# Kernel tuning notes

Hardware: AMD Instinct MI355X
Metric: run time of the kernel (lower is better)

The kernel has to match this reference:

```python
import jax, jax.numpy as jnp
import numpy as np

B, S, DIM, H = 2, 2048, 1024, 16
DH = DIM // H            # 64
G = DH // 4              # 16 quaternion groups per head
IQ = DIM // 4            # 256
ROPE_BASE = 10000.0
SCALE = DH ** -0.5


def qlinear(x, wr, wi, wj, wk, b):
    # x: [B,S,4*IQ]; strided quaternion components, exact combo from QuaternionLinear.forward
    xr, xi, xj, xk = x[..., 0::4], x[..., 1::4], x[..., 2::4], x[..., 3::4]
    o_r = xr @ wr.T - xi @ wi.T - xj @ wj.T - xk @ wk.T
    o_i = xi @ wr.T + xr @ wi.T + xk @ wk.T - xj @ wj.T
    o_j = xj @ wr.T - xk @ wk.T + xr @ wj.T + xi @ wi.T
    o_k = xk @ wr.T + xj @ wj.T - xi @ wi.T + xr @ wk.T
    out = jnp.stack([o_r, o_i, o_j, o_k], axis=-1).reshape(x.shape[:-1] + (-1,))
    return out + b


def qrope(x):
    # x: [B,H,S,DH]; left quaternion multiply u(theta) \otimes q, axis_mode='cycle'
    b, h, s, dh = x.shape
    g = dh // 4
    xq = x.reshape(b, h, s, g, 4)
    t = jnp.arange(s, dtype=x.dtype)
    inv = 1.0 / (ROPE_BASE ** (jnp.arange(g, dtype=x.dtype) / g))
    ang = t[:, None] * inv[None, :]            # [S,G]
    cos, sin = jnp.cos(ang), jnp.sin(ang)
    gi = jnp.arange(g)
    ax_i = (gi % 3 == 0).astype(x.dtype)
    ax_j = (gi % 3 == 1).astype(x.dtype)
    ax_k = (gi % 3 == 2).astype(x.dtype)
    ur, ui, uj, uk = cos, sin * ax_i, sin * ax_j, sin * ax_k   # [S,G] broadcast over [B,H,S,G]
    xr, xi, xj, xk = xq[..., 0], xq[..., 1], xq[..., 2], xq[..., 3]
    pr = ur * xr - ui * xi - uj * xj - uk * xk
    pi = ur * xi + ui * xr + uj * xk - uk * xj
    pj = ur * xj - ui * xk + uj * xr + uk * xi
    pk = ur * xk + ui * xj - uj * xi + uk * xr
    return jnp.stack([pr, pi, pj, pk], axis=-1).reshape(b, h, s, dh)


def setup_inputs() -> dict:
    key = jax.random.key(0)
    ks = jax.random.split(key, 24)
    x = jax.random.normal(ks[0], (B, S, DIM), dtype=jnp.float32)
    # causal mask: True = masked
    mask = jnp.broadcast_to(jnp.triu(jnp.ones((S, S), dtype=bool), k=1), (B, S, S))
    inp = {"x": x, "mask": mask}
    i = 1
    for proj in ("q", "k", "v", "o"):
        for comp in ("wr", "wi", "wj", "wk"):
            inp[f"{proj}_{comp}"] = jax.random.normal(ks[i], (IQ, IQ), dtype=jnp.float32) * 0.02
            i += 1
        inp[f"{proj}_b"] = jnp.zeros((DIM,), dtype=jnp.float32)
    return inp


def reference(x, mask,
              q_wr, q_wi, q_wj, q_wk, q_b,
              k_wr, k_wi, k_wj, k_wk, k_b,
              v_wr, v_wi, v_wj, v_wk, v_b,
              o_wr, o_wi, o_wj, o_wk, o_b):
    b, s, dm = x.shape
    q = qlinear(x, q_wr, q_wi, q_wj, q_wk, q_b).reshape(b, s, H, DH).transpose(0, 2, 1, 3)
    k = qlinear(x, k_wr, k_wi, k_wj, k_wk, k_b).reshape(b, s, H, DH).transpose(0, 2, 1, 3)
    v = qlinear(x, v_wr, v_wi, v_wj, v_wk, v_b).reshape(b, s, H, DH).transpose(0, 2, 1, 3)
    q, k = qrope(q), qrope(k)
    scores = jnp.einsum('bhsd,bhtd->bhst', q, k) * SCALE
    scores = jnp.where(mask[:, None, :, :], -jnp.inf, scores)
    a = jax.nn.softmax(scores, axis=-1)
    out = jnp.einsum('bhst,bhtd->bhsd', a, v).transpose(0, 2, 1, 3).reshape(b, s, dm)
    return qlinear(out, o_wr, o_wi, o_wj, o_wk, o_b)
```

## Files before the change

### kernel.cpp

```cpp
#include <hip/hip_runtime.h>
#include <stdint.h>

typedef unsigned short u16;
typedef unsigned int   u32;

#define NB   2
#define NS   2048
#define NDIM 1024
#define NH   16
#define NDH  64
#define QSCALE 0.18033688011112042f

typedef __bf16 bf16x8 __attribute__((ext_vector_type(8)));
typedef float  f32x4  __attribute__((ext_vector_type(4)));

#define MFMA_BF16(a,b,c) __builtin_amdgcn_mfma_f32_16x16x32_bf16((a),(b),(c),0,0,0)

#define XBF_OFF   (256)
#define WD_OFF    (XBF_OFF  + 8*1024*1024)
#define BIAS_OFF  (WD_OFF   + 8*1024*1024)
#define QB_OFF    (BIAS_OFF + 16384)
#define KB_OFF    (QB_OFF   + 8*1024*1024)
#define VT_OFF    (KB_OFF   + 8*1024*1024)
#define OP_OFF    (VT_OFF   + 8*1024*1024)
#define LP_OFF    (OP_OFF   + 16*1024*1024)

__device__ __forceinline__ float bf2f(u16 h){
  union { u32 u; float f; } v; v.u = ((u32)h) << 16; return v.f;
}
__device__ __forceinline__ u16 f2bf(float f){
  union { float f; u32 u; } v; v.f = f;
  u32 r = (v.u >> 16) & 1u;
  return (u16)((v.u + 0x7fffu + r) >> 16);
}
__device__ __forceinline__ float load_val(const void* p, int i, int isbf){
  return isbf ? bf2f(((const u16*)p)[i]) : ((const float*)p)[i];
}
__device__ __forceinline__ void gl_lds16(const u16* g, u16* l){
  __builtin_amdgcn_global_load_lds(
      (__attribute__((address_space(1))) void*)(uintptr_t)g,
      (__attribute__((address_space(3))) void*)(uintptr_t)l,
      16, 0, 0);
}

__global__ void detect_kernel(const u16* __restrict__ x, int* __restrict__ flag){
  __shared__ int cnt;
  if (threadIdx.x == 0) cnt = 0;
  __syncthreads();
  int ok = 0;
  int base = threadIdx.x * 16;
  for (int i = base; i < base + 16; ++i){
    u16 h = x[i];
    int e = (h >> 7) & 0xFF;
    if ((e > 96 && e < 158) || ((h & 0x7FFF) == 0)) ok++;
  }
  atomicAdd(&cnt, ok);
  __syncthreads();
  if (threadIdx.x == 0) *flag = (cnt > 3600) ? 1 : 0;
}

__global__ void conv_x_kernel(const void* __restrict__ xin, u16* __restrict__ xbf,
                              const int* __restrict__ flag){
  int isbf = *flag;
  int t = blockIdx.x * 256 + threadIdx.x;
  if (isbf){
    ((uint4*)xbf)[t] = ((const uint4*)xin)[t];
  } else {
    const float4* f4 = (const float4*)xin;
    float4 a = f4[2*t], b = f4[2*t+1];
    ushort4 lo = { f2bf(a.x), f2bf(a.y), f2bf(a.z), f2bf(a.w) };
    ushort4 hi = { f2bf(b.x), f2bf(b.y), f2bf(b.z), f2bf(b.w) };
    ((ushort4*)xbf)[2*t]   = lo;
    ((ushort4*)xbf)[2*t+1] = hi;
  }
}

struct QPtrs { const void* w[16]; const void* b[4]; };

__global__ void build_w_kernel(QPtrs ptrs, u16* __restrict__ wd,
                               float* __restrict__ biasf, const int* __restrict__ flag){
  int isbf = *flag;
  int idx = blockIdx.x * 256 + threadIdx.x;
  int n = idx & 255, m = (idx >> 8) & 255, c = (idx >> 16) & 3, p = idx >> 18;
  int src = m * 256 + n;
  float vr = load_val(ptrs.w[p*4+0], src, isbf);
  float vi = load_val(ptrs.w[p*4+1], src, isbf);
  float vj = load_val(ptrs.w[p*4+2], src, isbf);
  float vk = load_val(ptrs.w[p*4+3], src, isbf);
  float o0, o1, o2, o3;
  switch (c){
    case 0:  o0 = vr; o1 = -vi; o2 = -vj; o3 = -vk; break;
    case 1:  o0 = vi; o1 =  vr; o2 = -vj; o3 =  vk; break;
    case 2:  o0 = vj; o1 =  vi; o2 =  vr; o3 = -vk; break;
    default: o0 = vk; o1 = -vi; o2 =  vj; o3 =  vr; break;
  }
  ushort4 sv = { f2bf(o0), f2bf(o1), f2bf(o2), f2bf(o3) };
  *(ushort4*)&wd[(size_t)p * 1048576 + (size_t)(4*m + c) * 1024 + 4*n] = sv;
  if (idx < 4096){
    int pp = idx >> 10, oo = idx & 1023;
    biasf[idx] = load_val(ptrs.b[pp], oo, isbf);
  }
}

__global__ __launch_bounds__(256)
void gemm_qkv_kernel(const u16* __restrict__ A, const u16* __restrict__ Bw,
                     const float* __restrict__ bias,
                     u16* __restrict__ qb, u16* __restrict__ kb, u16* __restrict__ vt){
  __shared__ u16 sA[2][128 * 32];
  __shared__ u16 sB[2][128 * 32];
  int tid = threadIdx.x, w = tid >> 6, lane = tid & 63, quad = lane >> 4, l16 = lane & 15;
  int n0 = blockIdx.x * 128, m0 = blockIdx.y * 128;

  f32x4 acc[4][4];
#pragma unroll
  for (int i = 0; i < 4; ++i)
#pragma unroll
    for (int j = 0; j < 4; ++j) acc[i][j] = (f32x4){0.f, 0.f, 0.f, 0.f};

  int cp = lane & 3, rl = lane >> 2;
  int gc = (cp ^ ((rl >> 1) & 3)) * 8;
  const u16* ga = A  + (size_t)(m0 + w*16 + rl) * 1024 + gc;
  const u16* gb = Bw + (size_t)(n0 + w*16 + rl) * 1024 + gc;
  int ldo = w * 512 + lane * 8;
  int xorv = ((l16 >> 1) & 3) * 8;
  int mw = (w & 1) * 64, nw = (w >> 1) * 64;

  auto stage = [&](int k0, int b){
#pragma unroll
    for (int i = 0; i < 2; ++i){
      gl_lds16(ga + (size_t)i * 65536 + k0, &sA[b][ldo + i * 2048]);
      gl_lds16(gb + (size_t)i * 65536 + k0, &sB[b][ldo + i * 2048]);
    }
  };

  stage(0, 0);
  for (int it = 0; it < 32; ++it){
    __syncthreads();
    if (it < 31) stage((it + 1) * 32, (it + 1) & 1);
    const u16* cA = sA[it & 1];
    const u16* cB = sB[it & 1];
    bf16x8 af[4], bfr[4];
#pragma unroll
    for (int mt = 0; mt < 4; ++mt)
      af[mt] = *(const bf16x8*)&cA[(mw + mt*16 + l16) * 32 + (quad*8 ^ xorv)];
#pragma unroll
    for (int nt = 0; nt < 4; ++nt)
      bfr[nt] = *(const bf16x8*)&cB[(nw + nt*16 + l16) * 32 + (quad*8 ^ xorv)];
#pragma unroll
    for (int mt = 0; mt < 4; ++mt)
#pragma unroll
      for (int nt = 0; nt < 4; ++nt)
        acc[mt][nt] = MFMA_BF16(af[mt], bfr[nt], acc[mt][nt]);
  }

  int proj = n0 >> 10;
  if (proj == 2){
#pragma unroll
    for (int mt = 0; mt < 4; ++mt){
      int row = m0 + mw + mt*16 + quad*4;
      int b = row >> 11, seq0 = row & 2047;
#pragma unroll
      for (int nt = 0; nt < 4; ++nt){
        int col = n0 + nw + nt*16 + l16;
        int o = col & 1023, h = o >> 6, d = o & 63;
        float bv = bias[col];
        ushort4 pv = { f2bf(acc[mt][nt][0] + bv), f2bf(acc[mt][nt][1] + bv),
                       f2bf(acc[mt][nt][2] + bv), f2bf(acc[mt][nt][3] + bv) };
        *(ushort4*)&vt[((size_t)((b*16 + h) * 64 + d)) * 2048 + seq0] = pv;
      }
    }
  } else {
    float sc = (proj == 0) ? QSCALE : 1.0f;
    u16* dst = proj ? kb : qb;
    int c = l16 & 3;
#pragma unroll
    for (int nt = 0; nt < 4; ++nt){
      int col = n0 + nw + nt*16 + l16;
      int o = col & 1023, h = o >> 6, d = o & 63;
      int g = d >> 2;
      int ax = g % 3;
      int mask = ax + 1;
      int tbl = (ax == 0) ? 0xA : (ax == 1 ? 0x6 : 0xC);
      float sgn = ((tbl >> c) & 1) ? 1.f : -1.f;
      float inv = __builtin_amdgcn_exp2f(-(float)g * 0.8304820237218405f);
      float bv = bias[col];
#pragma unroll
      for (int mt = 0; mt < 4; ++mt){
        int row0 = m0 + mw + mt*16 + quad*4;
        int b = row0 >> 11, s0 = row0 & 2047;
        size_t obase = ((size_t)((b*16 + h) * 2048 + s0)) * 64 + d;
#pragma unroll
        for (int r = 0; r < 4; ++r){
          float v = acc[mt][nt][r] + bv;
          float vp = __shfl_xor(v, mask);
          float ang = (float)(s0 + r) * inv;
          float co = __cosf(ang) * sc;
          float si = __sinf(ang) * sc * sgn;
          dst[obase + (size_t)r * 64] = f2bf(co * v + si * vp);
        }
      }
    }
  }
}

__global__ __launch_bounds__(256)
void gemm_o_kernel(const u16* __restrict__ A, const u16* __restrict__ Bw,
                   const float* __restrict__ bias, void* __restrict__ dout,
                   const int* __restrict__ flag){
  __shared__ u16 sA[2][64 * 32];
  __shared__ u16 sB[2][128 * 32];
  int tid = threadIdx.x, w = tid >> 6, lane = tid & 63, quad = lane >> 4, l16 = lane & 15;
  int n0 = blockIdx.x * 128, m0 = blockIdx.y * 64;

  f32x4 acc[2][4];
#pragma unroll
  for (int i = 0; i < 2; ++i)
#pragma unroll
    for (int j = 0; j < 4; ++j) acc[i][j] = (f32x4){0.f, 0.f, 0.f, 0.f};

  int cp = lane & 3, rl = lane >> 2;
  int gc = (cp ^ ((rl >> 1) & 3)) * 8;
  int xorv = ((l16 >> 1) & 3) * 8;
  int mw = (w & 1) * 32, nw = (w >> 1) * 64;

  auto stage = [&](int k0, int b){
#pragma unroll
    for (int i = 0; i < 3; ++i){
      int ch = w * 3 + i;
      int lr = (ch < 4 ? ch : ch - 4) * 16 + rl;
      int eo = (ch < 4 ? ch : ch - 4) * 512 + lane * 8;
      if (ch < 4) gl_lds16(A  + (size_t)(m0 + lr) * 1024 + k0 + gc, &sA[b][eo]);
      else        gl_lds16(Bw + (size_t)(n0 + lr) * 1024 + k0 + gc, &sB[b][eo]);
    }
  };

  stage(0, 0);
  for (int it = 0; it < 32; ++it){
    __syncthreads();
    if (it < 31) stage((it + 1) * 32, (it + 1) & 1);
    const u16* cA = sA[it & 1];
    const u16* cB = sB[it & 1];
    bf16x8 af[2], bfr[4];
#pragma unroll
    for (int mt = 0; mt < 2; ++mt)
      af[mt] = *(const bf16x8*)&cA[(mw + mt*16 + l16) * 32 + (quad*8 ^ xorv)];
#pragma unroll
    for (int nt = 0; nt < 4; ++nt)
      bfr[nt] = *(const bf16x8*)&cB[(nw + nt*16 + l16) * 32 + (quad*8 ^ xorv)];
#pragma unroll
    for (int mt = 0; mt < 2; ++mt)
#pragma unroll
      for (int nt = 0; nt < 4; ++nt)
        acc[mt][nt] = MFMA_BF16(af[mt], bfr[nt], acc[mt][nt]);
  }

  int isbf = *flag;
#pragma unroll
  for (int mt = 0; mt < 2; ++mt){
    int row = m0 + mw + mt*16 + quad*4;
#pragma unroll
    for (int nt = 0; nt < 4; ++nt){
      int col = n0 + nw + nt*16 + l16;
      float bv = bias[col];
#pragma unroll
      for (int r = 0; r < 4; ++r){
        float val = acc[mt][nt][r] + bv;
        size_t addr = (size_t)(row + r) * 1024 + col;
        if (isbf) ((u16*)dout)[addr] = f2bf(val);
        else      ((float*)dout)[addr] = val;
      }
    }
  }
}

#define SPT 20

__global__ __launch_bounds__(256, 3)
void attn_kernel(const u16* __restrict__ Q, const u16* __restrict__ K,
                 const u16* __restrict__ Vt, u16* __restrict__ OP,
                 float* __restrict__ LP){
  __shared__ u16 sK[2][4096];
  __shared__ u16 sPT[4][64 * SPT];
  int bh  = blockIdx.x;
  int spl = blockIdx.y;
  int qt  = 15 - (int)blockIdx.z;
  int tid = threadIdx.x, w = tid >> 6, lane = tid & 63, quad = lane >> 4, l16 = lane & 15;
  size_t kbase = (size_t)bh * 2048 * 64;
  size_t vbase = (size_t)bh * 64 * 2048;
  int rowbase = qt * 128 + w * 32;
  u16* spw = &sPT[w][0];

  bf16x8 qf[2][2];
#pragma unroll
  for (int g = 0; g < 2; ++g)
#pragma unroll
    for (int kc = 0; kc < 2; ++kc)
      qf[g][kc] = *(const bf16x8*)(Q + kbase + (size_t)(rowbase + g*16 + l16) * 64 + kc*32 + quad*8);

  f32x4 oaccT[2][4];
  float lsum[2][4];
#pragma unroll
  for (int g = 0; g < 2; ++g)
#pragma unroll
    for (int i = 0; i < 4; ++i){ oaccT[g][i] = (f32x4){0.f,0.f,0.f,0.f}; lsum[g][i] = 0.f; }

  int kt0 = spl ? (qt + 1) : 0;
  int ntiles = qt + 1;

  auto stage = [&](int kt, int b){
    int kcol = kt * 64;
#pragma unroll
    for (int p = 0; p < 2; ++p){
      int slot = w*128 + p*64 + lane;
      int row = slot >> 3, dc = (slot & 7) ^ (row & 7);
      gl_lds16(K + kbase + (size_t)(kcol + row) * 64 + dc*8, &sK[b][(w*128 + p*64) * 8]);
    }
  };

  stage(kt0, 0);
  for (int i = 0; i < ntiles; ++i){
    int kcol = (kt0 + i) * 64;
    __syncthreads();
    if (i + 1 < ntiles) stage(kt0 + i + 1, (i + 1) & 1);
    const u16* bK = sK[i & 1];

    if (kcol <= rowbase + 31){
      bf16x8 vf[4][2];
#pragma unroll
      for (int dn = 0; dn < 4; ++dn)
#pragma unroll
        for (int kc = 0; kc < 2; ++kc)
          vf[dn][kc] = *(const bf16x8*)(Vt + vbase + (size_t)(dn*16 + l16) * 2048
                                        + kcol + kc*32 + quad*8);
      bf16x8 bk[2][4];
#pragma unroll
      for (int kc = 0; kc < 2; ++kc)
#pragma unroll
        for (int nt = 0; nt < 4; ++nt){
          int rw = nt*16 + l16;
          int ch = ((kc*4 + quad) ^ (rw & 7)) * 8;
          bk[kc][nt] = *(const bf16x8*)&bK[rw*64 + ch];
        }
#pragma unroll
      for (int g = 0; g < 2; ++g){
        int G0 = rowbase + g*16;
        if (kcol <= G0 + 15){
          f32x4 sacc[4];
#pragma unroll
          for (int nt = 0; nt < 4; ++nt) sacc[nt] = (f32x4){0.f,0.f,0.f,0.f};
#pragma unroll
          for (int kc = 0; kc < 2; ++kc)
#pragma unroll
            for (int nt = 0; nt < 4; ++nt)
              sacc[nt] = MFMA_BF16(qf[g][kc], bk[kc][nt], sacc[nt]);

          if (kcol + 63 > G0){
#pragma unroll
            for (int nt = 0; nt < 4; ++nt){
              int col = kcol + nt*16 + l16;
              ushort4 pv;
#pragma unroll
              for (int r = 0; r < 4; ++r){
                int row = G0 + quad*4 + r;
                float pp = (col <= row) ? __builtin_amdgcn_exp2f(sacc[nt][r]) : 0.f;
                lsum[g][r] += pp;
                ((u16*)&pv)[r] = f2bf(pp);
              }
              *(ushort4*)&spw[(nt*16 + l16) * SPT + quad*4] = pv;
            }
          } else {
#pragma unroll
            for (int nt = 0; nt < 4; ++nt){
              ushort4 pv;
#pragma unroll
              for (int r = 0; r < 4; ++r){
                float pp = __builtin_amdgcn_exp2f(sacc[nt][r]);
                lsum[g][r] += pp;
                ((u16*)&pv)[r] = f2bf(pp);
              }
              *(ushort4*)&spw[(nt*16 + l16) * SPT + quad*4] = pv;
            }
          }
#pragma unroll
          for (int kc = 0; kc < 2; ++kc){
            bf16x8 pf;
#pragma unroll
            for (int j = 0; j < 8; ++j)
              pf[j] = ((const __bf16*)spw)[(kc*32 + quad*8 + j) * SPT + l16];
#pragma unroll
            for (int dn = 0; dn < 4; ++dn)
              oaccT[g][dn] = MFMA_BF16(vf[dn][kc], pf, oaccT[g][dn]);
          }
        }
      }
    }
  }

  float* scr = (float*)spw;
#pragma unroll
  for (int g = 0; g < 2; ++g)
#pragma unroll
    for (int r = 0; r < 4; ++r){
      float l = lsum[g][r];
      l += __shfl_xor(l, 1); l += __shfl_xor(l, 2);
      l += __shfl_xor(l, 4); l += __shfl_xor(l, 8);
      if (l16 == 0) scr[g*16 + quad*4 + r] = l;
    }
  float lrow[2];
#pragma unroll
  for (int g = 0; g < 2; ++g) lrow[g] = scr[g*16 + l16];

  size_t obase = ((size_t)(spl*32 + bh)) * 2048;
#pragma unroll
  for (int g = 0; g < 2; ++g){
    int row = rowbase + g*16 + l16;
    if (quad == 0) LP[obase + row] = lrow[g];
#pragma unroll
    for (int dn = 0; dn < 4; ++dn){
      ushort4 ov = { f2bf(oaccT[g][dn][0]), f2bf(oaccT[g][dn][1]),
                     f2bf(oaccT[g][dn][2]), f2bf(oaccT[g][dn][3]) };
      *(ushort4*)&OP[(obase + row) * 64 + dn*16 + quad*4] = ov;
    }
  }
}

__global__ void combine_kernel(const u16* __restrict__ OP, const float* __restrict__ LP,
                               u16* __restrict__ Ab){
  int idx = blockIdx.x * 256 + threadIdx.x;
  int dc = idx & 7, s = (idx >> 3) & 2047, bh = idx >> 14;
  size_t r0 = (size_t)bh * 2048 + s, r1 = (size_t)(32 + bh) * 2048 + s;
  float invl = 1.f / (LP[r0] + LP[r1]);
  union { uint4 v; u16 h[8]; } a0, a1; ushort4 o[2];
  a0.v = *(const uint4*)&OP[r0 * 64 + dc*8];
  a1.v = *(const uint4*)&OP[r1 * 64 + dc*8];
#pragma unroll
  for (int p = 0; p < 2; ++p)
#pragma unroll
    for (int j = 0; j < 4; ++j)
      ((u16*)&o[p])[j] = f2bf((bf2f(a0.h[p*4+j]) + bf2f(a1.h[p*4+j])) * invl);
  int b = bh >> 4, h = bh & 15;
  u16* dst = &Ab[((size_t)(b*2048 + s)) * 1024 + h*64 + dc*8];
  *(ushort4*)dst = o[0];
  *(ushort4*)(dst + 4) = o[1];
}

extern "C" void kernel_launch(void* const* d_in, const int* in_sizes, int n_in,
                              void* d_out, int out_size, void* d_ws, size_t ws_size,
                              hipStream_t stream){
  (void)in_sizes; (void)n_in; (void)out_size; (void)ws_size;
  char* ws = (char*)d_ws;
  int*   flag  = (int*)ws;
  u16*   Xbf   = (u16*)(ws + XBF_OFF);
  u16*   Wd    = (u16*)(ws + WD_OFF);
  float* biasf = (float*)(ws + BIAS_OFF);
  u16*   Qb    = (u16*)(ws + QB_OFF);
  u16*   Kb    = (u16*)(ws + KB_OFF);
  u16*   Vt    = (u16*)(ws + VT_OFF);
  u16*   OP    = (u16*)(ws + OP_OFF);
  float* LP    = (float*)(ws + LP_OFF);
  u16*   Ab    = Xbf;

  detect_kernel<<<1, 256, 0, stream>>>((const u16*)d_in[0], flag);
  conv_x_kernel<<<2048, 256, 0, stream>>>(d_in[0], Xbf, flag);

  QPtrs ptrs;
  for (int p = 0; p < 4; ++p){
    for (int wi = 0; wi < 4; ++wi) ptrs.w[p*4 + wi] = d_in[2 + p*5 + wi];
    ptrs.b[p] = d_in[2 + p*5 + 4];
  }
  build_w_kernel<<<4096, 256, 0, stream>>>(ptrs, Wd, biasf, flag);

  gemm_qkv_kernel<<<dim3(24, 32), 256, 0, stream>>>(Xbf, Wd, biasf, Qb, Kb, Vt);
  attn_kernel<<<dim3(32, 2, 16), 256, 0, stream>>>(Qb, Kb, Vt, OP, LP);
  combine_kernel<<<2048, 256, 0, stream>>>(OP, LP, Ab);
  gemm_o_kernel<<<dim3(8, 64), 256, 0, stream>>>(Ab, Wd + 3*1048576, biasf + 3072,
                                                 d_out, flag);
}
```

Measured before the change: 254.3 us.

## Shrink GEMM tiles and load A fragments directly from global into registers

Both the QKV and output-projection GEMMs now use smaller M (and for O, N) tiles and double the grid size, with launch bounds raised to 4 blocks per SU. The A operand is no longer staged through LDS. Each wave loads its own MFMA A-fragment straight from global memory into registers and prefetches the next k-step into a second register set, while B stays double-buffered in LDS. The aim is more blocks for latency hiding and less LDS traffic and space, at the cost of less data reuse per tile and A reads that go uncoalesced or repeat across waves.

Result: slower. 284.4 us (+11.8%).

```diff
diff --git a/kernel.cpp b/kernel.cpp
--- a/kernel.cpp
+++ b/kernel.cpp
@@ -102,61 +102,68 @@
   }
 }
 
-__global__ __launch_bounds__(256)
+__global__ __launch_bounds__(256, 4)
 void gemm_qkv_kernel(const u16* __restrict__ A, const u16* __restrict__ Bw,
                      const float* __restrict__ bias,
                      u16* __restrict__ qb, u16* __restrict__ kb, u16* __restrict__ vt){
-  __shared__ u16 sA[2][128 * 32];
   __shared__ u16 sB[2][128 * 32];
   int tid = threadIdx.x, w = tid >> 6, lane = tid & 63, quad = lane >> 4, l16 = lane & 15;
-  int n0 = blockIdx.x * 128, m0 = blockIdx.y * 128;
-
-  f32x4 acc[4][4];
-#pragma unroll
-  for (int i = 0; i < 4; ++i)
+  int n0 = blockIdx.x * 128, m0 = blockIdx.y * 64;
+
+  f32x4 acc[2][4];
+#pragma unroll
+  for (int i = 0; i < 2; ++i)
 #pragma unroll
     for (int j = 0; j < 4; ++j) acc[i][j] = (f32x4){0.f, 0.f, 0.f, 0.f};
 
   int cp = lane & 3, rl = lane >> 2;
   int gc = (cp ^ ((rl >> 1) & 3)) * 8;
-  const u16* ga = A  + (size_t)(m0 + w*16 + rl) * 1024 + gc;
-  const u16* gb = Bw + (size_t)(n0 + w*16 + rl) * 1024 + gc;
-  int ldo = w * 512 + lane * 8;
   int xorv = ((l16 >> 1) & 3) * 8;
-  int mw = (w & 1) * 64, nw = (w >> 1) * 64;
-
-  auto stage = [&](int k0, int b){
+  int mw = (w & 1) * 32, nw = (w >> 1) * 64;
+
+  const u16* ga0 = A + (size_t)(m0 + mw + l16) * 1024 + quad * 8;
+
+  auto stageB = [&](int k0, int b){
 #pragma unroll
     for (int i = 0; i < 2; ++i){
-      gl_lds16(ga + (size_t)i * 65536 + k0, &sA[b][ldo + i * 2048]);
-      gl_lds16(gb + (size_t)i * 65536 + k0, &sB[b][ldo + i * 2048]);
+      int ch = w * 2 + i;
+      gl_lds16(Bw + (size_t)(n0 + ch*16 + rl) * 1024 + k0 + gc,
+               &sB[b][ch * 512 + lane * 8]);
     }
   };
 
-  stage(0, 0);
+  bf16x8 afc[2], afn[2];
+  stageB(0, 0);
+#pragma unroll
+  for (int mt = 0; mt < 2; ++mt)
+    afc[mt] = *(const bf16x8*)(ga0 + (size_t)mt * 16384);
+
   for (int it = 0; it < 32; ++it){
     __syncthreads();
-    if (it < 31) stage((it + 1) * 32, (it + 1) & 1);
-    const u16* cA = sA[it & 1];
+    if (it < 31){
+      stageB((it + 1) * 32, (it + 1) & 1);
+#pragma unroll
+      for (int mt = 0; mt < 2; ++mt)
+        afn[mt] = *(const bf16x8*)(ga0 + (size_t)mt * 16384 + (it + 1) * 32);
+    }
     const u16* cB = sB[it & 1];
-    bf16x8 af[4], bfr[4];
-#pragma unroll
-    for (int mt = 0; mt < 4; ++mt)
-      af[mt] = *(const bf16x8*)&cA[(mw + mt*16 + l16) * 32 + (quad*8 ^ xorv)];
+    bf16x8 bfr[4];
 #pragma unroll
     for (int nt = 0; nt < 4; ++nt)
       bfr[nt] = *(const bf16x8*)&cB[(nw + nt*16 + l16) * 32 + (quad*8 ^ xorv)];
 #pragma unroll
-    for (int mt = 0; mt < 4; ++mt)
+    for (int mt = 0; mt < 2; ++mt)
 #pragma unroll
       for (int nt = 0; nt < 4; ++nt)
-        acc[mt][nt] = MFMA_BF16(af[mt], bfr[nt], acc[mt][nt]);
+        acc[mt][nt] = MFMA_BF16(afc[mt], bfr[nt], acc[mt][nt]);
+#pragma unroll
+    for (int mt = 0; mt < 2; ++mt) afc[mt] = afn[mt];
   }
 
   int proj = n0 >> 10;
   if (proj == 2){
 #pragma unroll
-    for (int mt = 0; mt < 4; ++mt){
+    for (int mt = 0; mt < 2; ++mt){
       int row = m0 + mw + mt*16 + quad*4;
       int b = row >> 11, seq0 = row & 2047;
 #pragma unroll
@@ -185,7 +192,7 @@
       float inv = __builtin_amdgcn_exp2f(-(float)g * 0.8304820237218405f);
       float bv = bias[col];
 #pragma unroll
-      for (int mt = 0; mt < 4; ++mt){
+      for (int mt = 0; mt < 2; ++mt){
         int row0 = m0 + mw + mt*16 + quad*4;
         int b = row0 >> 11, s0 = row0 & 2047;
         size_t obase = ((size_t)((b*16 + h) * 2048 + s0)) * 64 + d;
@@ -203,55 +210,58 @@
   }
 }
 
-__global__ __launch_bounds__(256)
+__global__ __launch_bounds__(256, 4)
 void gemm_o_kernel(const u16* __restrict__ A, const u16* __restrict__ Bw,
                    const float* __restrict__ bias, void* __restrict__ dout,
                    const int* __restrict__ flag){
-  __shared__ u16 sA[2][64 * 32];
-  __shared__ u16 sB[2][128 * 32];
+  __shared__ u16 sB[2][64 * 32];
   int tid = threadIdx.x, w = tid >> 6, lane = tid & 63, quad = lane >> 4, l16 = lane & 15;
-  int n0 = blockIdx.x * 128, m0 = blockIdx.y * 64;
-
-  f32x4 acc[2][4];
+  int n0 = blockIdx.x * 64, m0 = blockIdx.y * 64;
+
+  f32x4 acc[2][2];
 #pragma unroll
   for (int i = 0; i < 2; ++i)
 #pragma unroll
-    for (int j = 0; j < 4; ++j) acc[i][j] = (f32x4){0.f, 0.f, 0.f, 0.f};
+    for (int j = 0; j < 2; ++j) acc[i][j] = (f32x4){0.f, 0.f, 0.f, 0.f};
 
   int cp = lane & 3, rl = lane >> 2;
   int gc = (cp ^ ((rl >> 1) & 3)) * 8;
   int xorv = ((l16 >> 1) & 3) * 8;
-  int mw = (w & 1) * 32, nw = (w >> 1) * 64;
-
-  auto stage = [&](int k0, int b){
-#pragma unroll
-    for (int i = 0; i < 3; ++i){
-      int ch = w * 3 + i;
-      int lr = (ch < 4 ? ch : ch - 4) * 16 + rl;
-      int eo = (ch < 4 ? ch : ch - 4) * 512 + lane * 8;
-      if (ch < 4) gl_lds16(A  + (size_t)(m0 + lr) * 1024 + k0 + gc, &sA[b][eo]);
-      else        gl_lds16(Bw + (size_t)(n0 + lr) * 1024 + k0 + gc, &sB[b][eo]);
-    }
+  int mw = (w & 1) * 32, nw = (w >> 1) * 32;
+
+  const u16* ga0 = A + (size_t)(m0 + mw + l16) * 1024 + quad * 8;
+
+  auto stageB = [&](int k0, int b){
+    gl_lds16(Bw + (size_t)(n0 + w*16 + rl) * 1024 + k0 + gc,
+             &sB[b][w * 512 + lane * 8]);
   };
 
-  stage(0, 0);
+  bf16x8 afc[2], afn[2];
+  stageB(0, 0);
+#pragma unroll
+  for (int mt = 0; mt < 2; ++mt)
+    afc[mt] = *(const bf16x8*)(ga0 + (size_t)mt * 16384);
+
   for (int it = 0; it < 32; ++it){
     __syncthreads();
-    if (it < 31) stage((it + 1) * 32, (it + 1) & 1);
-    const u16* cA = sA[it & 1];
+    if (it < 31){
+      stageB((it + 1) * 32, (it + 1) & 1);
+#pragma unroll
+      for (int mt = 0; mt < 2; ++mt)
+        afn[mt] = *(const bf16x8*)(ga0 + (size_t)mt * 16384 + (it + 1) * 32);
+    }
     const u16* cB = sB[it & 1];
-    bf16x8 af[2], bfr[4];
+    bf16x8 bfr[2];
+#pragma unroll
+    for (int nt = 0; nt < 2; ++nt)
+      bfr[nt] = *(const bf16x8*)&cB[(nw + nt*16 + l16) * 32 + (quad*8 ^ xorv)];
 #pragma unroll
     for (int mt = 0; mt < 2; ++mt)
-      af[mt] = *(const bf16x8*)&cA[(mw + mt*16 + l16) * 32 + (quad*8 ^ xorv)];
-#pragma unroll
-    for (int nt = 0; nt < 4; ++nt)
-      bfr[nt] = *(const bf16x8*)&cB[(nw + nt*16 + l16) * 32 + (quad*8 ^ xorv)];
-#pragma unroll
-    for (int mt = 0; mt < 2; ++mt)
-#pragma unroll
-      for (int nt = 0; nt < 4; ++nt)
-        acc[mt][nt] = MFMA_BF16(af[mt], bfr[nt], acc[mt][nt]);
+#pragma unroll
+      for (int nt = 0; nt < 2; ++nt)
+        acc[mt][nt] = MFMA_BF16(afc[mt], bfr[nt], acc[mt][nt]);
+#pragma unroll
+    for (int mt = 0; mt < 2; ++mt) afc[mt] = afn[mt];
   }
 
   int isbf = *flag;
@@ -259,7 +269,7 @@
   for (int mt = 0; mt < 2; ++mt){
     int row = m0 + mw + mt*16 + quad*4;
 #pragma unroll
-    for (int nt = 0; nt < 4; ++nt){
+    for (int nt = 0; nt < 2; ++nt){
       int col = n0 + nw + nt*16 + l16;
       float bv = bias[col];
 #pragma unroll
@@ -470,9 +480,9 @@
   }
   build_w_kernel<<<4096, 256, 0, stream>>>(ptrs, Wd, biasf, flag);
 
-  gemm_qkv_kernel<<<dim3(24, 32), 256, 0, stream>>>(Xbf, Wd, biasf, Qb, Kb, Vt);
+  gemm_qkv_kernel<<<dim3(24, 64), 256, 0, stream>>>(Xbf, Wd, biasf, Qb, Kb, Vt);
   attn_kernel<<<dim3(32, 2, 16), 256, 0, stream>>>(Qb, Kb, Vt, OP, LP);
   combine_kernel<<<2048, 256, 0, stream>>>(OP, LP, Ab);
-  gemm_o_kernel<<<dim3(8, 64), 256, 0, stream>>>(Ab, Wd + 3*1048576, biasf + 3072,
-                                                 d_out, flag);
-}
+  gemm_o_kernel<<<dim3(16, 64), 256, 0, stream>>>(Ab, Wd + 3*1048576, biasf + 3072,
+                                                  d_out, flag);
+}
```

## Load QKV GEMM fragments directly from global memory into registers, dropping LDS staging

Applied to the files above, without the earlier changes.

Replaces the LDS double-buffered tiles in the QKV projection GEMM with direct global loads of MFMA fragments into registers, prefetching the next k-step while the current one computes. This removes the per-iteration __syncthreads and the LDS traffic. In exchange, data is no longer shared across waves, so each A/B row is fetched by two waves from global/L2. The per-lane 16-byte loads are also less coalesced than before, and register pressure goes up.

New measurement: 297.7 us. +17.1%, slower.

```diff
diff --git a/kernel.cpp b/kernel.cpp
--- a/kernel.cpp
+++ b/kernel.cpp
@@ -106,10 +106,9 @@
 void gemm_qkv_kernel(const u16* __restrict__ A, const u16* __restrict__ Bw,
                      const float* __restrict__ bias,
                      u16* __restrict__ qb, u16* __restrict__ kb, u16* __restrict__ vt){
-  __shared__ u16 sA[2][128 * 32];
-  __shared__ u16 sB[2][128 * 32];
   int tid = threadIdx.x, w = tid >> 6, lane = tid & 63, quad = lane >> 4, l16 = lane & 15;
   int n0 = blockIdx.x * 128, m0 = blockIdx.y * 128;
+  int mw = (w & 1) * 64, nw = (w >> 1) * 64;
 
   f32x4 acc[4][4];
 #pragma unroll
@@ -117,40 +116,33 @@
 #pragma unroll
     for (int j = 0; j < 4; ++j) acc[i][j] = (f32x4){0.f, 0.f, 0.f, 0.f};
 
-  int cp = lane & 3, rl = lane >> 2;
-  int gc = (cp ^ ((rl >> 1) & 3)) * 8;
-  const u16* ga = A  + (size_t)(m0 + w*16 + rl) * 1024 + gc;
-  const u16* gb = Bw + (size_t)(n0 + w*16 + rl) * 1024 + gc;
-  int ldo = w * 512 + lane * 8;
-  int xorv = ((l16 >> 1) & 3) * 8;
-  int mw = (w & 1) * 64, nw = (w >> 1) * 64;
-
-  auto stage = [&](int k0, int b){
-#pragma unroll
-    for (int i = 0; i < 2; ++i){
-      gl_lds16(ga + (size_t)i * 65536 + k0, &sA[b][ldo + i * 2048]);
-      gl_lds16(gb + (size_t)i * 65536 + k0, &sB[b][ldo + i * 2048]);
-    }
-  };
-
-  stage(0, 0);
+  const u16* pa = A  + (size_t)(m0 + mw + l16) * 1024 + quad * 8;
+  const u16* pb = Bw + (size_t)(n0 + nw + l16) * 1024 + quad * 8;
+
+  bf16x8 afc[4], bfc[4], afn[4], bfn[4];
+#pragma unroll
+  for (int t = 0; t < 4; ++t){
+    afc[t] = *(const bf16x8*)(pa + (size_t)t * 16384);
+    bfc[t] = *(const bf16x8*)(pb + (size_t)t * 16384);
+  }
+
+#pragma unroll 2
   for (int it = 0; it < 32; ++it){
-    __syncthreads();
-    if (it < 31) stage((it + 1) * 32, (it + 1) & 1);
-    const u16* cA = sA[it & 1];
-    const u16* cB = sB[it & 1];
-    bf16x8 af[4], bfr[4];
+    if (it < 31){
+      int k1 = (it + 1) * 32;
+#pragma unroll
+      for (int t = 0; t < 4; ++t){
+        afn[t] = *(const bf16x8*)(pa + (size_t)t * 16384 + k1);
+        bfn[t] = *(const bf16x8*)(pb + (size_t)t * 16384 + k1);
+      }
+    }
 #pragma unroll
     for (int mt = 0; mt < 4; ++mt)
-      af[mt] = *(const bf16x8*)&cA[(mw + mt*16 + l16) * 32 + (quad*8 ^ xorv)];
-#pragma unroll
-    for (int nt = 0; nt < 4; ++nt)
-      bfr[nt] = *(const bf16x8*)&cB[(nw + nt*16 + l16) * 32 + (quad*8 ^ xorv)];
-#pragma unroll
-    for (int mt = 0; mt < 4; ++mt)
 #pragma unroll
       for (int nt = 0; nt < 4; ++nt)
-        acc[mt][nt] = MFMA_BF16(af[mt], bfr[nt], acc[mt][nt]);
+        acc[mt][nt] = MFMA_BF16(afc[mt], bfc[nt], acc[mt][nt]);
+#pragma unroll
+    for (int t = 0; t < 4; ++t){ afc[t] = afn[t]; bfc[t] = bfn[t]; }
   }
 
   int proj = n0 >> 10;
```

## Fuse split-attention combine into output GEMM and merge prep kernels

Applied to the files above, without the earlier changes.

Folds the detect, convert-x and build-weight kernels into one prep kernel that does per-block dtype detection, removing two launches and a serial detection pass. Also removes the combine kernel: the output-projection GEMM now reads the two partial attention outputs and their row sums directly, normalises them while staging its A tile into padded LDS, and so skips an intermediate activation round-trip through memory. The price is that A staging in the GEMM becomes register-mediated global loads plus ALU work instead of async global-to-LDS copies, and 8 GEMM column blocks redo the same combine for each row tile.

New measurement: 259.3 us. No clear change (+2.0%).

```diff
diff --git a/kernel.cpp b/kernel.cpp
--- a/kernel.cpp
+++ b/kernel.cpp
@@ -42,63 +42,68 @@
       (__attribute__((address_space(3))) void*)(uintptr_t)l,
       16, 0, 0);
 }
-
-__global__ void detect_kernel(const u16* __restrict__ x, int* __restrict__ flag){
+__device__ __forceinline__ int sane16(u16 h){
+  int e = (h >> 7) & 0xFF;
+  return ((e > 96 && e < 158) || ((h & 0x7FFF) == 0)) ? 1 : 0;
+}
+
+struct QPtrs { const void* w[16]; const void* b[4]; };
+
+__global__ void prep_kernel(const void* __restrict__ xin, u16* __restrict__ xbf,
+                            QPtrs ptrs, u16* __restrict__ wd,
+                            float* __restrict__ biasf, int* __restrict__ flag){
   __shared__ int cnt;
-  if (threadIdx.x == 0) cnt = 0;
+  int bx = blockIdx.x, tid = threadIdx.x;
+  if (tid == 0) cnt = 0;
   __syncthreads();
-  int ok = 0;
-  int base = threadIdx.x * 16;
-  for (int i = base; i < base + 16; ++i){
-    u16 h = x[i];
-    int e = (h >> 7) & 0xFF;
-    if ((e > 96 && e < 158) || ((h & 0x7FFF) == 0)) ok++;
-  }
-  atomicAdd(&cnt, ok);
-  __syncthreads();
-  if (threadIdx.x == 0) *flag = (cnt > 3600) ? 1 : 0;
-}
-
-__global__ void conv_x_kernel(const void* __restrict__ xin, u16* __restrict__ xbf,
-                              const int* __restrict__ flag){
-  int isbf = *flag;
-  int t = blockIdx.x * 256 + threadIdx.x;
-  if (isbf){
-    ((uint4*)xbf)[t] = ((const uint4*)xin)[t];
+
+  if (bx < 2048){
+    int t = bx * 256 + tid;
+    uint4 v = ((const uint4*)xin)[t];
+    const u16* hv = (const u16*)&v;
+    int ok = 0;
+#pragma unroll
+    for (int j = 0; j < 8; ++j) ok += sane16(hv[j]);
+    atomicAdd(&cnt, ok);
+    __syncthreads();
+    int isbf = (cnt > 1700) ? 1 : 0;
+    if (bx == 0 && tid == 0) *flag = isbf;
+    if (isbf){
+      ((uint4*)xbf)[t] = v;
+    } else {
+      const float4* f4 = (const float4*)xin;
+      float4 a = f4[2*t], b = f4[2*t+1];
+      ushort4 lo = { f2bf(a.x), f2bf(a.y), f2bf(a.z), f2bf(a.w) };
+      ushort4 hi = { f2bf(b.x), f2bf(b.y), f2bf(b.z), f2bf(b.w) };
+      ((ushort4*)xbf)[2*t]   = lo;
+      ((ushort4*)xbf)[2*t+1] = hi;
+    }
   } else {
-    const float4* f4 = (const float4*)xin;
-    float4 a = f4[2*t], b = f4[2*t+1];
-    ushort4 lo = { f2bf(a.x), f2bf(a.y), f2bf(a.z), f2bf(a.w) };
-    ushort4 hi = { f2bf(b.x), f2bf(b.y), f2bf(b.z), f2bf(b.w) };
-    ((ushort4*)xbf)[2*t]   = lo;
-    ((ushort4*)xbf)[2*t+1] = hi;
-  }
-}
-
-struct QPtrs { const void* w[16]; const void* b[4]; };
-
-__global__ void build_w_kernel(QPtrs ptrs, u16* __restrict__ wd,
-                               float* __restrict__ biasf, const int* __restrict__ flag){
-  int isbf = *flag;
-  int idx = blockIdx.x * 256 + threadIdx.x;
-  int n = idx & 255, m = (idx >> 8) & 255, c = (idx >> 16) & 3, p = idx >> 18;
-  int src = m * 256 + n;
-  float vr = load_val(ptrs.w[p*4+0], src, isbf);
-  float vi = load_val(ptrs.w[p*4+1], src, isbf);
-  float vj = load_val(ptrs.w[p*4+2], src, isbf);
-  float vk = load_val(ptrs.w[p*4+3], src, isbf);
-  float o0, o1, o2, o3;
-  switch (c){
-    case 0:  o0 = vr; o1 = -vi; o2 = -vj; o3 = -vk; break;
-    case 1:  o0 = vi; o1 =  vr; o2 = -vj; o3 =  vk; break;
-    case 2:  o0 = vj; o1 =  vi; o2 =  vr; o3 = -vk; break;
-    default: o0 = vk; o1 = -vi; o2 =  vj; o3 =  vr; break;
-  }
-  ushort4 sv = { f2bf(o0), f2bf(o1), f2bf(o2), f2bf(o3) };
-  *(ushort4*)&wd[(size_t)p * 1048576 + (size_t)(4*m + c) * 1024 + 4*n] = sv;
-  if (idx < 4096){
-    int pp = idx >> 10, oo = idx & 1023;
-    biasf[idx] = load_val(ptrs.b[pp], oo, isbf);
+    int idx = (bx - 2048) * 256 + tid;
+    int n = idx & 255, m = (idx >> 8) & 255, c = (idx >> 16) & 3, p = idx >> 18;
+    const u16* probe = (const u16*)ptrs.w[p*4];
+    int ok = sane16(probe[tid]) + sane16(probe[tid + 256]);
+    atomicAdd(&cnt, ok);
+    __syncthreads();
+    int isbf = (cnt > 450) ? 1 : 0;
+    int src = m * 256 + n;
+    float vr = load_val(ptrs.w[p*4+0], src, isbf);
+    float vi = load_val(ptrs.w[p*4+1], src, isbf);
+    float vj = load_val(ptrs.w[p*4+2], src, isbf);
+    float vk = load_val(ptrs.w[p*4+3], src, isbf);
+    float o0, o1, o2, o3;
+    switch (c){
+      case 0:  o0 = vr; o1 = -vi; o2 = -vj; o3 = -vk; break;
+      case 1:  o0 = vi; o1 =  vr; o2 = -vj; o3 =  vk; break;
+      case 2:  o0 = vj; o1 =  vi; o2 =  vr; o3 = -vk; break;
+      default: o0 = vk; o1 = -vi; o2 =  vj; o3 =  vr; break;
+    }
+    ushort4 sv = { f2bf(o0), f2bf(o1), f2bf(o2), f2bf(o3) };
+    *(ushort4*)&wd[(size_t)p * 1048576 + (size_t)(4*m + c) * 1024 + 4*n] = sv;
+    if (idx < 4096){
+      int pp = idx >> 10, oo = idx & 1023;
+      biasf[idx] = load_val(ptrs.b[pp], oo, isbf);
+    }
   }
 }
 
@@ -204,10 +209,10 @@
 }
 
 __global__ __launch_bounds__(256)
-void gemm_o_kernel(const u16* __restrict__ A, const u16* __restrict__ Bw,
-                   const float* __restrict__ bias, void* __restrict__ dout,
-                   const int* __restrict__ flag){
-  __shared__ u16 sA[2][64 * 32];
+void gemm_o_kernel(const u16* __restrict__ OP, const float* __restrict__ LP,
+                   const u16* __restrict__ Bw, const float* __restrict__ bias,
+                   void* __restrict__ dout, const int* __restrict__ flag){
+  __shared__ u16 sA[2][64 * 40];
   __shared__ u16 sB[2][128 * 32];
   int tid = threadIdx.x, w = tid >> 6, lane = tid & 63, quad = lane >> 4, l16 = lane & 15;
   int n0 = blockIdx.x * 128, m0 = blockIdx.y * 64;
@@ -219,31 +224,51 @@
     for (int j = 0; j < 4; ++j) acc[i][j] = (f32x4){0.f, 0.f, 0.f, 0.f};
 
   int cp = lane & 3, rl = lane >> 2;
-  int gc = (cp ^ ((rl >> 1) & 3)) * 8;
+  int gcB = (cp ^ ((rl >> 1) & 3)) * 8;
   int xorv = ((l16 >> 1) & 3) * 8;
   int mw = (w & 1) * 32, nw = (w >> 1) * 64;
 
-  auto stage = [&](int k0, int b){
-#pragma unroll
-    for (int i = 0; i < 3; ++i){
-      int ch = w * 3 + i;
-      int lr = (ch < 4 ? ch : ch - 4) * 16 + rl;
-      int eo = (ch < 4 ? ch : ch - 4) * 512 + lane * 8;
-      if (ch < 4) gl_lds16(A  + (size_t)(m0 + lr) * 1024 + k0 + gc, &sA[b][eo]);
-      else        gl_lds16(Bw + (size_t)(n0 + lr) * 1024 + k0 + gc, &sB[b][eo]);
+  int am = m0 + w*16 + rl;
+  int ab = am >> 11, as = am & 2047;
+
+  auto stageB = [&](int k0, int b){
+#pragma unroll
+    for (int i = 0; i < 2; ++i){
+      int c = w * 2 + i;
+      gl_lds16(Bw + (size_t)(n0 + c*16 + rl) * 1024 + k0 + gcB,
+               &sB[b][c * 512 + lane * 8]);
     }
   };
-
-  stage(0, 0);
+  auto stageA = [&](int k0, int b){
+    int kk = k0 + cp * 8;
+    int h = kk >> 6, d = kk & 63;
+    size_t r0 = (size_t)(ab*16 + h) * 2048 + as;
+    size_t r1 = r0 + 65536;
+    union { uint4 v; u16 s[8]; } a0, a1;
+    a0.v = *(const uint4*)&OP[r0 * 64 + d];
+    a1.v = *(const uint4*)&OP[r1 * 64 + d];
+    float invl = 1.f / (LP[r0] + LP[r1]);
+    union { uint4 v; u16 s[8]; } o;
+#pragma unroll
+    for (int j = 0; j < 8; ++j)
+      o.s[j] = f2bf((bf2f(a0.s[j]) + bf2f(a1.s[j])) * invl);
+    *(uint4*)&sA[b][(w*16 + rl) * 40 + cp * 8] = o.v;
+  };
+
+  stageB(0, 0);
+  stageA(0, 0);
   for (int it = 0; it < 32; ++it){
     __syncthreads();
-    if (it < 31) stage((it + 1) * 32, (it + 1) & 1);
+    if (it < 31){
+      stageB((it + 1) * 32, (it + 1) & 1);
+      stageA((it + 1) * 32, (it + 1) & 1);
+    }
     const u16* cA = sA[it & 1];
     const u16* cB = sB[it & 1];
     bf16x8 af[2], bfr[4];
 #pragma unroll
     for (int mt = 0; mt < 2; ++mt)
-      af[mt] = *(const bf16x8*)&cA[(mw + mt*16 + l16) * 32 + (quad*8 ^ xorv)];
+      af[mt] = *(const bf16x8*)&cA[(mw + mt*16 + l16) * 40 + quad * 8];
 #pragma unroll
     for (int nt = 0; nt < 4; ++nt)
       bfr[nt] = *(const bf16x8*)&cB[(nw + nt*16 + l16) * 32 + (quad*8 ^ xorv)];
@@ -424,26 +449,6 @@
   }
 }
 
-__global__ void combine_kernel(const u16* __restrict__ OP, const float* __restrict__ LP,
-                               u16* __restrict__ Ab){
-  int idx = blockIdx.x * 256 + threadIdx.x;
-  int dc = idx & 7, s = (idx >> 3) & 2047, bh = idx >> 14;
-  size_t r0 = (size_t)bh * 2048 + s, r1 = (size_t)(32 + bh) * 2048 + s;
-  float invl = 1.f / (LP[r0] + LP[r1]);
-  union { uint4 v; u16 h[8]; } a0, a1; ushort4 o[2];
-  a0.v = *(const uint4*)&OP[r0 * 64 + dc*8];
-  a1.v = *(const uint4*)&OP[r1 * 64 + dc*8];
-#pragma unroll
-  for (int p = 0; p < 2; ++p)
-#pragma unroll
-    for (int j = 0; j < 4; ++j)
-      ((u16*)&o[p])[j] = f2bf((bf2f(a0.h[p*4+j]) + bf2f(a1.h[p*4+j])) * invl);
-  int b = bh >> 4, h = bh & 15;
-  u16* dst = &Ab[((size_t)(b*2048 + s)) * 1024 + h*64 + dc*8];
-  *(ushort4*)dst = o[0];
-  *(ushort4*)(dst + 4) = o[1];
-}
-
 extern "C" void kernel_launch(void* const* d_in, const int* in_sizes, int n_in,
                               void* d_out, int out_size, void* d_ws, size_t ws_size,
                               hipStream_t stream){
@@ -458,21 +463,16 @@
   u16*   Vt    = (u16*)(ws + VT_OFF);
   u16*   OP    = (u16*)(ws + OP_OFF);
   float* LP    = (float*)(ws + LP_OFF);
-  u16*   Ab    = Xbf;
-
-  detect_kernel<<<1, 256, 0, stream>>>((const u16*)d_in[0], flag);
-  conv_x_kernel<<<2048, 256, 0, stream>>>(d_in[0], Xbf, flag);
 
   QPtrs ptrs;
   for (int p = 0; p < 4; ++p){
     for (int wi = 0; wi < 4; ++wi) ptrs.w[p*4 + wi] = d_in[2 + p*5 + wi];
     ptrs.b[p] = d_in[2 + p*5 + 4];
   }
-  build_w_kernel<<<4096, 256, 0, stream>>>(ptrs, Wd, biasf, flag);
-
+
+  prep_kernel<<<6144, 256, 0, stream>>>(d_in[0], Xbf, ptrs, Wd, biasf, flag);
   gemm_qkv_kernel<<<dim3(24, 32), 256, 0, stream>>>(Xbf, Wd, biasf, Qb, Kb, Vt);
   attn_kernel<<<dim3(32, 2, 16), 256, 0, stream>>>(Qb, Kb, Vt, OP, LP);
-  combine_kernel<<<2048, 256, 0, stream>>>(OP, LP, Ab);
-  gemm_o_kernel<<<dim3(8, 64), 256, 0, stream>>>(Ab, Wd + 3*1048576, biasf + 3072,
+  gemm_o_kernel<<<dim3(8, 64), 256, 0, stream>>>(OP, LP, Wd + 3*1048576, biasf + 3072,
                                                  d_out, flag);
 }
```
